# Kernel optimization log

Measured on AMD Instinct MI355X. Metric: run time of the kernel, lower is better.

Reference implementation:

```python
import math
import jax, jax.numpy as jnp
from jax import lax
import numpy as np

B, M, L = 256, 21, 512
P, S, D = 16, 8, 256
NL, EXP, H, LAM = 3, 2, 96, 0.01
T = (L - P) // S + 1  # 63 patches
HID = D * EXP


def _pos_enc():
    pe = np.zeros((T, D), np.float32)
    pos = np.arange(T, dtype=np.float32)[:, None]
    div = np.exp(np.arange(0, D, 2, dtype=np.float32) * (-math.log(10000.0) / D))
    pe[:, 0::2] = np.sin(pos * div)
    pe[:, 1::2] = np.cos(pos * div)
    return jnp.asarray(pe)


def _clin(zr, zi, Wr, Wi, br, bi):
    # faithful to torch: bias br added to both terms of yr (cancels), bi added twice in yi
    yr = (zr @ Wr.T + br) - (zi @ Wi.T + br)
    yi = (zr @ Wi.T + bi) + (zi @ Wr.T + bi)
    return yr, yi


def _softshrink(zr, zi):
    mag = jnp.sqrt(zr * zr + zi * zi)
    scale = jnp.maximum(mag - LAM, 0.0) / (mag + 1e-8) * (mag > LAM).astype(zr.dtype)
    return zr * scale, zi * scale


def _layernorm(x, g, b):
    mu = jnp.mean(x, -1, keepdims=True)
    var = jnp.mean((x - mu) ** 2, -1, keepdims=True)
    return (x - mu) / jnp.sqrt(var + 1e-5) * g + b


def _block(x, p):
    (Tw, Tb, Gew, Geb, Gpw, Gpb,
     H1Wr, H1Wi, H1br, H1bi, H2Wr, H2Wi, H2br, H2bi, lng, lnb) = p
    g = jax.nn.gelu(x @ Gew.T + Geb, approximate=False) @ Gpw.T + Gpb
    zf = jnp.fft.rfft(x, axis=1)  # FFT along time/patch axis T
    zr, zi = zf.real, zf.imag
    zr, zi = _clin(zr, zi, H1Wr, H1Wi, H1br, H1bi)
    zr, zi = _softshrink(zr, zi)
    zr, zi = _clin(zr, zi, H2Wr, H2Wi, H2br, H2bi)
    pt = jnp.fft.irfft(lax.complex(zr, zi), n=x.shape[1], axis=1)
    out = (g * pt) @ Tw.T + Tb
    return _layernorm(out + x, lng, lnb)


def _forward(x, conv_w, conv_b, tp, sp, gate_w, gate_b, proj_w, proj_b):
    # per-instance, per-variable norm over time (biased std, eps on std)
    mean = jnp.mean(x, -1, keepdims=True)
    std = jnp.sqrt(jnp.mean((x - mean) ** 2, -1, keepdims=True))
    xn = (x - mean) / (std + 1e-5)
    patches = lax.conv_general_dilated(xn, conv_w, (S,), 'VALID',
                                       dimension_numbers=('NCH', 'OIH', 'NCH'))
    patches = patches + conv_b[None, :, None]
    h = patches.transpose(0, 2, 1) + _pos_enc()[None]  # (B, T, D)
    t = h
    s = h
    for i in range(NL):
        t = _block(t, tuple(a[i] for a in tp))
        s = _block(s, tuple(a[i] for a in sp))
    gate = jax.nn.sigmoid(t @ gate_w.T + gate_b)
    feat = gate * t + (1.0 - gate) * s
    out = feat.reshape(feat.shape[0], -1) @ proj_w.T + proj_b
    y = out.reshape(-1, M, H) * (std + 1e-5) + mean
    return y


def setup_inputs() -> dict:
    key = jax.random.key(0)
    ks = iter(jax.random.split(key, 64))

    def nrm(shape, scale):
        return jax.random.normal(next(ks), shape, jnp.float32) * scale

    inp = {'x': nrm((B, M, L), 1.0)}
    inp['conv_w'] = nrm((D, M, P), 1.0 / math.sqrt(M * P))
    inp['conv_b'] = jnp.zeros((D,), jnp.float32)

    def layer_params(prefix):
        d = {}
        d[prefix + 'Tw'] = nrm((NL, D, D), 1.0 / math.sqrt(D))
        d[prefix + 'Tb'] = jnp.zeros((NL, D), jnp.float32)
        d[prefix + 'Gew'] = nrm((NL, HID, D), 1.0 / math.sqrt(D))
        d[prefix + 'Geb'] = jnp.zeros((NL, HID), jnp.float32)
        d[prefix + 'Gpw'] = nrm((NL, D, HID), 1.0 / math.sqrt(HID))
        d[prefix + 'Gpb'] = jnp.zeros((NL, D), jnp.float32)
        for hname in ('H1', 'H2'):
            d[prefix + hname + 'Wr'] = nrm((NL, D, D), 1.0 / math.sqrt(D))
            d[prefix + hname + 'Wi'] = nrm((NL, D, D), 1.0 / math.sqrt(D))
            d[prefix + hname + 'br'] = jnp.zeros((NL, D), jnp.float32)
            d[prefix + hname + 'bi'] = jnp.zeros((NL, D), jnp.float32)
        d[prefix + 'lng'] = jnp.ones((NL, D), jnp.float32)
        d[prefix + 'lnb'] = jnp.zeros((NL, D), jnp.float32)
        return d

    inp.update(layer_params('t_'))
    inp.update(layer_params('s_'))
    inp['gate_w'] = nrm((1, D), 1.0 / math.sqrt(D))
    inp['gate_b'] = jnp.zeros((1,), jnp.float32)
    inp['proj_w'] = nrm((M * H, T * D), 1.0 / math.sqrt(T * D))
    inp['proj_b'] = jnp.zeros((M * H,), jnp.float32)
    return inp


def reference(x, conv_w, conv_b,
              t_Tw, t_Tb, t_Gew, t_Geb, t_Gpw, t_Gpb,
              t_H1Wr, t_H1Wi, t_H1br, t_H1bi, t_H2Wr, t_H2Wi, t_H2br, t_H2bi, t_lng, t_lnb,
              s_Tw, s_Tb, s_Gew, s_Geb, s_Gpw, s_Gpb,
              s_H1Wr, s_H1Wi, s_H1br, s_H1bi, s_H2Wr, s_H2Wi, s_H2br, s_H2bi, s_lng, s_lnb,
              gate_w, gate_b, proj_w, proj_b):
    tp = (t_Tw, t_Tb, t_Gew, t_Geb, t_Gpw, t_Gpb,
          t_H1Wr, t_H1Wi, t_H1br, t_H1bi, t_H2Wr, t_H2Wi, t_H2br, t_H2bi, t_lng, t_lnb)
    sp = (s_Tw, s_Tb, s_Gew, s_Geb, s_Gpw, s_Gpb,
          s_H1Wr, s_H1Wi, s_H1br, s_H1bi, s_H2Wr, s_H2Wi, s_H2br, s_H2bi, s_lng, s_lnb)
    return _forward(x, conv_w, conv_b, tp, sp, gate_w, gate_b, proj_w, proj_b)
```

## Files before the change

kernel.cpp:

```cpp
#include <hip/hip_runtime.h>
#include <cstddef>
#include <cstdint>

#define B_    256
#define M_    21
#define L_    512
#define D_    256
#define T_    63
#define F_    32
#define NT_   16128
#define HID_  512
#define KCP_  352
#define H_    96
#define LAM_  0.01f
#define PZ_   12

typedef __attribute__((ext_vector_type(8))) short short8;
typedef __attribute__((ext_vector_type(4))) float f32x4;
typedef unsigned int u32;
typedef const u32 __attribute__((address_space(1)))* gas1_t;
typedef u32 __attribute__((address_space(3)))* las3_t;

__device__ __forceinline__ void async_copy16(const void* g, void* l) {
  __builtin_amdgcn_global_load_lds((gas1_t)g, (las3_t)(uintptr_t)l, 16, 0, 0);
}
__device__ __forceinline__ unsigned short f2bf(float x) {
  unsigned u = __float_as_uint(x);
  return (unsigned short)((u + 0x7FFF + ((u >> 16) & 1)) >> 16);
}
__device__ __forceinline__ float bf2f(unsigned short u) {
  return __uint_as_float(((unsigned)u) << 16);
}
__device__ __forceinline__ float gelu_exact(float v) {
  return 0.5f * v * (1.0f + erff(v * 0.70710678118654752f));
}
__device__ __forceinline__ float block_sum256(float v, float* red4) {
  #pragma unroll
  for (int off = 32; off > 0; off >>= 1) v += __shfl_down(v, off, 64);
  if ((threadIdx.x & 63) == 0) red4[threadIdx.x >> 6] = v;
  __syncthreads();
  float r = red4[0] + red4[1] + red4[2] + red4[3];
  __syncthreads();
  return r;
}
__device__ __forceinline__ float wave_sum(float v) {
  #pragma unroll
  for (int off = 1; off < 64; off <<= 1) v += __shfl_xor(v, off, 64);
  return v;
}

struct CvtEnt { const float* src; unsigned short* dst; int rows, scol, dcol, blk0; };
struct CvtArgs { CvtEnt e[19]; int nent; };
__global__ __launch_bounds__(256) void wprep_kernel(CvtArgs a) {
  int blk = blockIdx.x, e = 0;
  while (e + 1 < a.nent && a.e[e + 1].blk0 <= blk) ++e;
  CvtEnt en = a.e[e];
  int idx = (blk - en.blk0) * 256 + threadIdx.x;
  int total = en.rows * en.dcol;
  if (idx >= total) return;
  int r = idx / en.dcol, c = idx - r * en.dcol;
  float v = (c < en.scol) ? en.src[(size_t)r * en.scol + c] : 0.f;
  en.dst[idx] = f2bf(v);
}

struct CatArgs { const float* wr[12]; const float* wi[12]; };
__global__ __launch_bounds__(256) void wcat_kernel(CatArgs a, unsigned short* dst) {
  int e = blockIdx.x >> 10;
  int idx = ((blockIdx.x & 1023) << 8) + threadIdx.x;
  int r = idx >> 9, c = idx & 511;
  int cp = r >> 1, p = r & 1, d = c >> 1, q = c & 1;
  const float* wr = a.wr[e];
  const float* wi = a.wi[e];
  float v;
  if (p == 0) v = (q == 0) ? wr[cp * 256 + d] : -wi[cp * 256 + d];
  else        v = (q == 0) ? wi[cp * 256 + d] :  wr[cp * 256 + d];
  dst[(size_t)e * 262144 + idx] = f2bf(v);
}

template <int ACT, int OUTBF, int BIASM, int KSTEPS, int CVTA, int CVTW,
          int SHRINK, int MULPT, int SPLITK>
__global__ __launch_bounds__(256) void mm_kernel(
    const void* __restrict__ Av,
    const unsigned short* __restrict__ W0, const unsigned short* __restrict__ W1,
    const float* __restrict__ Wf,
    const float* __restrict__ b0, const float* __restrict__ b1,
    const unsigned short* __restrict__ ptb,
    void* __restrict__ Cv,
    const int K, const int Dout, const int ksteps_rt, const int yhalf, const int prow) {
  __shared__ __align__(16) unsigned short As[128 * 32];
  __shared__ __align__(16) unsigned short Bs[128 * 32];
  const int ksteps = KSTEPS ? KSTEPS : ksteps_rt;
  const int tid = threadIdx.x, w = tid >> 6, lane = tid & 63;
  const int quad = lane >> 4, r16 = lane & 15;
  const int kst = SPLITK ? (int)blockIdx.z * ksteps * 32 : 0;
  const int tower = ((int)blockIdx.y >= yhalf) ? 1 : 0;
  const unsigned short* Wb = tower ? W1 : W0;
  const float* bias = tower ? b1 : b0;

  const unsigned short* Ab = (const unsigned short*)Av;
  const float* Af = (const float*)Av;
  const unsigned short* gA = nullptr;
  unsigned short* lA = As + (w * 32) * 32;
  if (!CVTA) gA = Ab + (size_t)(blockIdx.y * 128 + w * 32 + (lane >> 2)) * K
                     + kst + (lane & 3) * 8;
  const unsigned short* gB = nullptr;
  unsigned short* lB = Bs + (w * 32) * 32;
  if (!CVTW) gB = Wb + (size_t)(blockIdx.x * 128 + w * 32 + (lane >> 2)) * K
                     + kst + (lane & 3) * 8;

  f32x4 acc[4][4];
  #pragma unroll
  for (int i = 0; i < 4; ++i)
    #pragma unroll
    for (int j = 0; j < 4; ++j)
      #pragma unroll
      for (int r = 0; r < 4; ++r) acc[i][j][r] = 0.f;

  for (int ks = 0; ks < ksteps; ++ks) {
    if (!CVTA) {
      async_copy16(gA, lA);
      async_copy16(gA + (size_t)16 * K, lA + 16 * 32);
      gA += 32;
    } else {
      int rowA = tid >> 1, halfk = (tid & 1) << 4;
      const float* asrc = Af + (size_t)((int)blockIdx.y * 128 + rowA) * K + ks * 32 + halfk;
      union { unsigned short u[16]; uint4 q[2]; } pk;
      #pragma unroll
      for (int n = 0; n < 16; n += 4) {
        float4 v = *reinterpret_cast<const float4*>(asrc + n);
        pk.u[n] = f2bf(v.x); pk.u[n + 1] = f2bf(v.y);
        pk.u[n + 2] = f2bf(v.z); pk.u[n + 3] = f2bf(v.w);
      }
      uint4* ad = reinterpret_cast<uint4*>(As + rowA * 32 + halfk);
      ad[0] = pk.q[0]; ad[1] = pk.q[1];
    }
    if (!CVTW) {
      async_copy16(gB, lB);
      async_copy16(gB + (size_t)16 * K, lB + 16 * 32);
      gB += 32;
    } else {
      int rowW = tid >> 1, halfk = (tid & 1) << 4;
      int wrow = blockIdx.x * 128 + rowW;
      if (wrow >= Dout) wrow = Dout - 1;
      const float* wsrc = Wf + (size_t)wrow * K + kst + ks * 32 + halfk;
      union { unsigned short u[16]; uint4 q[2]; } pk;
      #pragma unroll
      for (int n = 0; n < 16; n += 4) {
        float4 v = *reinterpret_cast<const float4*>(wsrc + n);
        pk.u[n] = f2bf(v.x); pk.u[n + 1] = f2bf(v.y);
        pk.u[n + 2] = f2bf(v.z); pk.u[n + 3] = f2bf(v.w);
      }
      uint4* bd = reinterpret_cast<uint4*>(Bs + rowW * 32 + halfk);
      bd[0] = pk.q[0]; bd[1] = pk.q[1];
    }
    __syncthreads();
    const unsigned short* pa = As + (64 * (w >> 1) + r16) * 32 + quad * 8;
    const unsigned short* pb = Bs + (64 * (w & 1) + r16) * 32 + quad * 8;
    short8 af[4], bfv[4];
    #pragma unroll
    for (int i = 0; i < 4; ++i) af[i] = *reinterpret_cast<const short8*>(pa + i * 512);
    #pragma unroll
    for (int j = 0; j < 4; ++j) bfv[j] = *reinterpret_cast<const short8*>(pb + j * 512);
    #pragma unroll
    for (int i = 0; i < 4; ++i)
      #pragma unroll
      for (int j = 0; j < 4; ++j)
        acc[i][j] = __builtin_amdgcn_mfma_f32_16x16x32_bf16(af[i], bfv[j], acc[i][j], 0, 0, 0);
    __syncthreads();
  }

  float* Cf = (float*)Cv;
  unsigned short* Cb = (unsigned short*)Cv;
  if (SPLITK) Cf += (size_t)blockIdx.z * prow * Dout;
  const int colb = blockIdx.x * 128 + 64 * (w & 1) + r16;
  const int rowb = blockIdx.y * 128 + 64 * (w >> 1) + quad * 4;
  #pragma unroll
  for (int j = 0; j < 4; ++j) {
    int col = colb + 16 * j;
    float bv = 0.f;
    if (BIASM == 0) bv = bias[col];
    else if (BIASM == 1) bv = (col & 1) ? 2.0f * bias[col >> 1] : 0.f;
    bool colok = (BIASM != 2) || (col < Dout);
    #pragma unroll
    for (int i = 0; i < 4; ++i) {
      #pragma unroll
      for (int r = 0; r < 4; ++r) {
        int row = rowb + 16 * i + r;
        float v = acc[i][j][r] + bv;
        if (ACT == 1) v = gelu_exact(v);
        if (SHRINK) {
          float o = __shfl_xor(v, 1, 64);
          float mag = sqrtf(v * v + o * o);
          float s = (mag > LAM_) ? (mag - LAM_) / (mag + 1e-8f) : 0.f;
          v *= s;
        }
        if (MULPT) v *= bf2f(ptb[(size_t)row * Dout + col]);
        if (colok) {
          if (OUTBF) Cb[(size_t)row * Dout + col] = f2bf(v);
          else       Cf[(size_t)row * Dout + col] = v;
        }
      }
    }
  }
}

__global__ __launch_bounds__(256) void norm_kernel(const float* __restrict__ x,
    float* __restrict__ xn, float* __restrict__ meanb, float* __restrict__ stdb) {
  __shared__ float red[4];
  int bm = blockIdx.x;
  const float* xr = x + (size_t)bm * L_;
  float v0 = xr[threadIdx.x], v1 = xr[threadIdx.x + 256];
  float mu = block_sum256(v0 + v1, red) * (1.0f / L_);
  float d0 = v0 - mu, d1 = v1 - mu;
  float sd = sqrtf(block_sum256(d0 * d0 + d1 * d1, red) * (1.0f / L_));
  float inv = 1.0f / (sd + 1e-5f);
  float* xo = xn + (size_t)bm * L_;
  xo[threadIdx.x] = d0 * inv;
  xo[threadIdx.x + 256] = d1 * inv;
  if (threadIdx.x == 0) { meanb[bm] = mu; stdb[bm] = sd; }
}

__global__ __launch_bounds__(256) void im2col_kernel(const float* __restrict__ xn,
                                                     unsigned short* __restrict__ im) {
  int row = blockIdx.x;
  int b = row / T_, t = row - b * T_;
  const float* xb = xn + (size_t)b * M_ * L_ + t * 8;
  unsigned short* o = im + (size_t)row * KCP_;
  for (int i = threadIdx.x; i < KCP_; i += 256) {
    float v = 0.f;
    if (i < 336) { int m = i >> 4, p = i & 15; v = xb[m * L_ + p]; }
    o[i] = f2bf(v);
  }
}

__global__ __launch_bounds__(256) void add_pe_kernel(const float* __restrict__ g0,
                                                     float* __restrict__ x32) {
  int row = blockIdx.x, d = threadIdx.x;
  int t = row % T_;
  size_t idx = (size_t)row * D_ + d;
  float freq = expf((float)(d & ~1) * (-9.210340371976184f / 256.0f));
  float ang = (float)t * freq;
  float pe = (d & 1) ? cosf(ang) : sinf(ang);
  float h = g0[idx] + pe;
  x32[idx] = h;
  x32[idx + (size_t)NT_ * D_] = h;
}

__global__ __launch_bounds__(256) void dft_kernel(const float* __restrict__ X,
                                                  unsigned short* __restrict__ Zcat) {
  __shared__ float2 tw[T_ * F_];
  int bt = blockIdx.x, d = threadIdx.x;
  for (int i = threadIdx.x; i < T_ * F_; i += 256) {
    int t = i >> 5, f = i & 31;
    int k = (f * t) % T_;
    float sn, cs;
    sincosf((6.283185307179586f / 63.0f) * (float)k, &sn, &cs);
    tw[i] = make_float2(cs, -sn);
  }
  __syncthreads();
  const float* xb = X + (size_t)bt * T_ * D_ + d;
  float ar[F_], ai[F_];
  #pragma unroll
  for (int f = 0; f < F_; ++f) { ar[f] = 0.f; ai[f] = 0.f; }
  for (int t = 0; t < T_; ++t) {
    float v = xb[(size_t)t * D_];
    const float2* w = &tw[t * F_];
    #pragma unroll
    for (int f = 0; f < F_; ++f) {
      float2 c = w[f];
      ar[f] = fmaf(v, c.x, ar[f]);
      ai[f] = fmaf(v, c.y, ai[f]);
    }
  }
  u32* z = reinterpret_cast<u32*>(Zcat + (size_t)bt * F_ * 512);
  #pragma unroll
  for (int f = 0; f < F_; ++f)
    z[f * 256 + d] = (u32)f2bf(ar[f]) | ((u32)f2bf(ai[f]) << 16);
}

__global__ __launch_bounds__(256) void irfft_kernel(const float* __restrict__ Y,
                                                    unsigned short* __restrict__ ptb) {
  __shared__ float2 tw[T_ * 31];
  int bt = blockIdx.x, d = threadIdx.x;
  for (int i = threadIdx.x; i < T_ * 31; i += 256) {
    int t = i / 31, f = i - t * 31 + 1;
    int k = (f * t) % T_;
    float sn, cs;
    sincosf((6.283185307179586f / 63.0f) * (float)k, &sn, &cs);
    tw[i] = make_float2(cs * (2.0f / 63.0f), -sn * (2.0f / 63.0f));
  }
  __syncthreads();
  const float* yb = Y + (size_t)bt * F_ * 512 + 2 * d;
  float y0 = yb[0] * (1.0f / 63.0f);
  float yr[31], yi[31];
  #pragma unroll
  for (int f = 1; f < F_; ++f) {
    float2 p = *reinterpret_cast<const float2*>(yb + (size_t)f * 512);
    yr[f - 1] = p.x;
    yi[f - 1] = p.y;
  }
  unsigned short* po = ptb + (size_t)bt * T_ * D_ + d;
  for (int t = 0; t < T_; ++t) {
    const float2* w = &tw[t * 31];
    float acc0 = y0, acc1 = 0.f;
    #pragma unroll
    for (int f = 0; f < 31; f += 2) {
      float2 c = w[f];
      acc0 = fmaf(yr[f], c.x, fmaf(yi[f], c.y, acc0));
      if (f + 1 < 31) {
        float2 c1 = w[f + 1];
        acc1 = fmaf(yr[f + 1], c1.x, fmaf(yi[f + 1], c1.y, acc1));
      }
    }
    po[(size_t)t * D_] = f2bf(acc0 + acc1);
  }
}

__global__ __launch_bounds__(256) void ln_kernel(const float* __restrict__ outb,
    float* __restrict__ x, const float* __restrict__ g0, const float* __restrict__ b0,
    const float* __restrict__ g1, const float* __restrict__ b1, int yhalf) {
  int row = blockIdx.x * 4 + (threadIdx.x >> 6);
  int lane = threadIdx.x & 63;
  const float* g = (row >= yhalf) ? g1 : g0;
  const float* b = (row >= yhalf) ? b1 : b0;
  size_t base = (size_t)row * D_ + lane * 4;
  float4 ov = *reinterpret_cast<const float4*>(outb + base);
  float4 xv = *reinterpret_cast<const float4*>(x + base);
  float v0 = ov.x + xv.x, v1 = ov.y + xv.y, v2 = ov.z + xv.z, v3 = ov.w + xv.w;
  float mu = wave_sum(v0 + v1 + v2 + v3) * (1.0f / D_);
  v0 -= mu; v1 -= mu; v2 -= mu; v3 -= mu;
  float var = wave_sum(v0 * v0 + v1 * v1 + v2 * v2 + v3 * v3) * (1.0f / D_);
  float is = rsqrtf(var + 1e-5f);
  float4 gv = *reinterpret_cast<const float4*>(g + lane * 4);
  float4 bv = *reinterpret_cast<const float4*>(b + lane * 4);
  float4 o;
  o.x = v0 * is * gv.x + bv.x;
  o.y = v1 * is * gv.y + bv.y;
  o.z = v2 * is * gv.z + bv.z;
  o.w = v3 * is * gv.w + bv.w;
  *reinterpret_cast<float4*>(x + base) = o;
}

__global__ __launch_bounds__(256) void gate_feat_kernel(const float* __restrict__ x32,
    const float* __restrict__ gw, const float* __restrict__ gb,
    unsigned short* __restrict__ featbf) {
  __shared__ float red[4];
  size_t base = (size_t)blockIdx.x * D_;
  int d = threadIdx.x;
  float tv = x32[base + d];
  float sv = x32[base + (size_t)NT_ * D_ + d];
  float gsum = block_sum256(tv * gw[d], red) + gb[0];
  float gate = 1.0f / (1.0f + expf(-gsum));
  featbf[base + d] = f2bf(gate * tv + (1.0f - gate) * sv);
}

__global__ __launch_bounds__(256) void final_kernel(const float* __restrict__ part,
    const float* __restrict__ pb, const float* __restrict__ stdb,
    const float* __restrict__ meanb, float* __restrict__ y) {
  int i = blockIdx.x * 256 + threadIdx.x;
  float acc = 0.f;
  #pragma unroll
  for (int z = 0; z < PZ_; ++z) acc += part[(size_t)z * 516096 + i];
  int b = i / 2016;
  int col = i - b * 2016;
  int m = col / H_;
  float sc = stdb[b * M_ + m] + 1e-5f;
  y[i] = (acc + pb[col]) * sc + meanb[b * M_ + m];
}

extern "C" void kernel_launch(void* const* d_in, const int* in_sizes, int n_in,
                              void* d_out, int out_size, void* d_ws, size_t ws_size,
                              hipStream_t stream) {
  const float* x      = (const float*)d_in[0];
  const float* conv_w = (const float*)d_in[1];
  const float* conv_b = (const float*)d_in[2];
  const float* tP[16];
  const float* sP[16];
  for (int i = 0; i < 16; ++i) tP[i] = (const float*)d_in[3 + i];
  for (int i = 0; i < 16; ++i) sP[i] = (const float*)d_in[19 + i];
  const float* gate_w = (const float*)d_in[35];
  const float* gate_b = (const float*)d_in[36];
  const float* proj_w = (const float*)d_in[37];
  const float* proj_b = (const float*)d_in[38];
  float* out = (float*)d_out;

  float* ws    = (float*)d_ws;
  float* x32   = ws;
  unsigned short* wb = (unsigned short*)(x32 + 8257536);
  float* meanb = x32 + 8257536 + 2600960;
  float* stdb  = meanb + 5376;
  float* R1    = stdb + 5376 + 16;
  float* R2    = R1 + 8388608;

  unsigned short* im2colB = (unsigned short*)R1;
  unsigned short* Zcat    = (unsigned short*)R1;
  unsigned short* Ycat1   = (unsigned short*)(R1 + 4194304);
  unsigned short* ptb     = (unsigned short*)(R1 + 4194304);
  unsigned short* gp      = (unsigned short*)R1;
  unsigned short* featbf  = (unsigned short*)R1;

  float* xn     = R2;
  float* g0buf  = R2;
  float* Ycat2f = R2;
  unsigned short* hidB = (unsigned short*)R2;
  float* outb   = R2;
  float* part   = R2;

  unsigned short* convW = wb;
  unsigned short* sets  = wb + 90112;
  unsigned short* catW  = wb + 90112 + 1966080;

  CvtArgs ca; int blk0 = 0, ne = 0;
  auto add_ent = [&](const float* s, unsigned short* d, int rows, int scol, int dcol) {
    ca.e[ne].src = s; ca.e[ne].dst = d; ca.e[ne].rows = rows;
    ca.e[ne].scol = scol; ca.e[ne].dcol = dcol; ca.e[ne].blk0 = blk0;
    blk0 += (rows * dcol + 255) / 256; ++ne;
  };
  add_ent(conv_w, convW, 256, 336, 352);
  for (int tw = 0; tw < 2; ++tw) {
    const float** Pp = tw ? (const float**)sP : (const float**)tP;
    for (int l = 0; l < 3; ++l) {
      unsigned short* sb = sets + (size_t)(tw * 3 + l) * 327680;
      add_ent(Pp[2] + (size_t)l * 131072, sb,          512, 256, 256);
      add_ent(Pp[4] + (size_t)l * 131072, sb + 131072, 256, 512, 512);
      add_ent(Pp[0] + (size_t)l * 65536,  sb + 262144, 256, 256, 256);
    }
  }
  ca.nent = ne;
  wprep_kernel<<<blk0, 256, 0, stream>>>(ca);

  CatArgs cat;
  for (int tw = 0; tw < 2; ++tw) {
    const float** Pp = tw ? (const float**)sP : (const float**)tP;
    for (int l = 0; l < 3; ++l) {
      int e0 = (tw * 3 + l) * 2;
      cat.wr[e0]     = Pp[6]  + (size_t)l * 65536;
      cat.wi[e0]     = Pp[7]  + (size_t)l * 65536;
      cat.wr[e0 + 1] = Pp[10] + (size_t)l * 65536;
      cat.wi[e0 + 1] = Pp[11] + (size_t)l * 65536;
    }
  }
  wcat_kernel<<<12 * 1024, 256, 0, stream>>>(cat, catW);

  norm_kernel<<<B_ * M_, 256, 0, stream>>>(x, xn, meanb, stdb);
  im2col_kernel<<<NT_, 256, 0, stream>>>(xn, im2colB);
  mm_kernel<0, 0, 0, 11, 0, 0, 0, 0, 0><<<dim3(2, 126), 256, 0, stream>>>(
      im2colB, convW, convW, nullptr, conv_b, conv_b, nullptr, g0buf,
      KCP_, 256, 0, 1 << 30, 0);
  add_pe_kernel<<<NT_, 256, 0, stream>>>(g0buf, x32);

  for (int l = 0; l < 3; ++l) {
    unsigned short* st0 = sets + (size_t)l * 327680;
    unsigned short* st1 = sets + (size_t)(3 + l) * 327680;
    unsigned short* c1t0 = catW + (size_t)((0 + l) * 2) * 262144;
    unsigned short* c2t0 = c1t0 + 262144;
    unsigned short* c1t1 = catW + (size_t)((3 + l) * 2) * 262144;
    unsigned short* c2t1 = c1t1 + 262144;

    dft_kernel<<<2 * B_, 256, 0, stream>>>(x32, Zcat);
    mm_kernel<0, 1, 1, 16, 0, 0, 1, 0, 0><<<dim3(4, 128), 256, 0, stream>>>(
        Zcat, c1t0, c1t1, nullptr, tP[9] + (size_t)l * D_, sP[9] + (size_t)l * D_,
        nullptr, Ycat1, 512, 512, 0, 64, 0);
    mm_kernel<0, 0, 1, 16, 0, 0, 0, 0, 0><<<dim3(4, 128), 256, 0, stream>>>(
        Ycat1, c2t0, c2t1, nullptr, tP[13] + (size_t)l * D_, sP[13] + (size_t)l * D_,
        nullptr, Ycat2f, 512, 512, 0, 64, 0);
    irfft_kernel<<<2 * B_, 256, 0, stream>>>(Ycat2f, ptb);
    mm_kernel<1, 1, 0, 8, 1, 0, 0, 0, 0><<<dim3(4, 252), 256, 0, stream>>>(
        x32, st0, st1, nullptr, tP[3] + (size_t)l * HID_, sP[3] + (size_t)l * HID_,
        nullptr, hidB, 256, 512, 0, 126, 0);
    mm_kernel<0, 1, 0, 16, 0, 0, 0, 1, 0><<<dim3(2, 252), 256, 0, stream>>>(
        hidB, st0 + 131072, st1 + 131072, nullptr,
        tP[5] + (size_t)l * D_, sP[5] + (size_t)l * D_, ptb, gp, 512, 256, 0, 126, 0);
    mm_kernel<0, 0, 0, 8, 0, 0, 0, 0, 0><<<dim3(2, 252), 256, 0, stream>>>(
        gp, st0 + 262144, st1 + 262144, nullptr,
        tP[1] + (size_t)l * D_, sP[1] + (size_t)l * D_, nullptr, outb, 256, 256, 0, 126, 0);
    ln_kernel<<<2 * NT_ / 4, 256, 0, stream>>>(outb, x32,
        tP[14] + (size_t)l * D_, tP[15] + (size_t)l * D_,
        sP[14] + (size_t)l * D_, sP[15] + (size_t)l * D_, NT_);
  }

  gate_feat_kernel<<<NT_, 256, 0, stream>>>(x32, gate_w, gate_b, featbf);
  mm_kernel<0, 0, 2, 0, 0, 1, 0, 0, 1><<<dim3(16, 2, PZ_), 256, 0, stream>>>(
      featbf, nullptr, nullptr, proj_w, nullptr, nullptr, nullptr, part,
      NT_, 2016, 504 / PZ_, 1 << 30, 256);
  final_kernel<<<2016, 256, 0, stream>>>(part, proj_b, stdb, meanb, out);
}
```

Measured before the change: 1.067 ms.

## Deepen GEMM K-tile to 64, store second spectral GEMM in bf16, vectorize gate kernel

```diff
diff --git a/kernel.cpp b/kernel.cpp
--- a/kernel.cpp
+++ b/kernel.cpp
@@ -13,7 +13,7 @@
 #define KCP_  352
 #define H_    96
 #define LAM_  0.01f
-#define PZ_   12
+#define PZ_   14
 
 typedef __attribute__((ext_vector_type(8))) short short8;
 typedef __attribute__((ext_vector_type(4))) float f32x4;
@@ -78,7 +78,7 @@
 }
 
 template <int ACT, int OUTBF, int BIASM, int KSTEPS, int CVTA, int CVTW,
-          int SHRINK, int MULPT, int SPLITK>
+          int SHRINK, int MULPT, int SPLITK, int BK>
 __global__ __launch_bounds__(256) void mm_kernel(
     const void* __restrict__ Av,
     const unsigned short* __restrict__ W0, const unsigned short* __restrict__ W1,
@@ -87,12 +87,13 @@
     const unsigned short* __restrict__ ptb,
     void* __restrict__ Cv,
     const int K, const int Dout, const int ksteps_rt, const int yhalf, const int prow) {
-  __shared__ __align__(16) unsigned short As[128 * 32];
-  __shared__ __align__(16) unsigned short Bs[128 * 32];
+  constexpr int NP = BK / 32;
+  __shared__ __align__(16) unsigned short As[NP * 128 * 32];
+  __shared__ __align__(16) unsigned short Bs[NP * 128 * 32];
   const int ksteps = KSTEPS ? KSTEPS : ksteps_rt;
   const int tid = threadIdx.x, w = tid >> 6, lane = tid & 63;
   const int quad = lane >> 4, r16 = lane & 15;
-  const int kst = SPLITK ? (int)blockIdx.z * ksteps * 32 : 0;
+  const int kst = SPLITK ? (int)blockIdx.z * ksteps * BK : 0;
   const int tower = ((int)blockIdx.y >= yhalf) ? 1 : 0;
   const unsigned short* Wb = tower ? W1 : W0;
   const float* bias = tower ? b1 : b0;
@@ -107,6 +108,8 @@
   unsigned short* lB = Bs + (w * 32) * 32;
   if (!CVTW) gB = Wb + (size_t)(blockIdx.x * 128 + w * 32 + (lane >> 2)) * K
                      + kst + (lane & 3) * 8;
+  const int crow = tid >> 3;
+  const int ck4  = (tid & 7) << 2;
 
   f32x4 acc[4][4];
   #pragma unroll
@@ -118,54 +121,62 @@
 
   for (int ks = 0; ks < ksteps; ++ks) {
     if (!CVTA) {
-      async_copy16(gA, lA);
-      async_copy16(gA + (size_t)16 * K, lA + 16 * 32);
-      gA += 32;
+      #pragma unroll
+      for (int p = 0; p < NP; ++p) {
+        async_copy16(gA + p * 32, lA + p * 4096);
+        async_copy16(gA + (size_t)16 * K + p * 32, lA + p * 4096 + 16 * 32);
+      }
+      gA += BK;
     } else {
-      int rowA = tid >> 1, halfk = (tid & 1) << 4;
-      const float* asrc = Af + (size_t)((int)blockIdx.y * 128 + rowA) * K + ks * 32 + halfk;
-      union { unsigned short u[16]; uint4 q[2]; } pk;
-      #pragma unroll
-      for (int n = 0; n < 16; n += 4) {
-        float4 v = *reinterpret_cast<const float4*>(asrc + n);
-        pk.u[n] = f2bf(v.x); pk.u[n + 1] = f2bf(v.y);
-        pk.u[n + 2] = f2bf(v.z); pk.u[n + 3] = f2bf(v.w);
+      #pragma unroll
+      for (int p = 0; p < NP; ++p)
+        #pragma unroll
+        for (int rr = 0; rr < 4; ++rr) {
+          int row128 = crow + 32 * rr;
+          const float* asrc = Af + (size_t)((int)blockIdx.y * 128 + row128) * K
+                                 + ks * BK + p * 32 + ck4;
+          float4 v = *reinterpret_cast<const float4*>(asrc);
+          ushort4 o; o.x = f2bf(v.x); o.y = f2bf(v.y); o.z = f2bf(v.z); o.w = f2bf(v.w);
+          *reinterpret_cast<ushort4*>(As + p * 4096 + row128 * 32 + ck4) = o;
+        }
+    }
+    if (!CVTW) {
+      #pragma unroll
+      for (int p = 0; p < NP; ++p) {
+        async_copy16(gB + p * 32, lB + p * 4096);
+        async_copy16(gB + (size_t)16 * K + p * 32, lB + p * 4096 + 16 * 32);
       }
-      uint4* ad = reinterpret_cast<uint4*>(As + rowA * 32 + halfk);
-      ad[0] = pk.q[0]; ad[1] = pk.q[1];
-    }
-    if (!CVTW) {
-      async_copy16(gB, lB);
-      async_copy16(gB + (size_t)16 * K, lB + 16 * 32);
-      gB += 32;
+      gB += BK;
     } else {
-      int rowW = tid >> 1, halfk = (tid & 1) << 4;
-      int wrow = blockIdx.x * 128 + rowW;
-      if (wrow >= Dout) wrow = Dout - 1;
-      const float* wsrc = Wf + (size_t)wrow * K + kst + ks * 32 + halfk;
-      union { unsigned short u[16]; uint4 q[2]; } pk;
-      #pragma unroll
-      for (int n = 0; n < 16; n += 4) {
-        float4 v = *reinterpret_cast<const float4*>(wsrc + n);
-        pk.u[n] = f2bf(v.x); pk.u[n + 1] = f2bf(v.y);
-        pk.u[n + 2] = f2bf(v.z); pk.u[n + 3] = f2bf(v.w);
-      }
-      uint4* bd = reinterpret_cast<uint4*>(Bs + rowW * 32 + halfk);
-      bd[0] = pk.q[0]; bd[1] = pk.q[1];
+      #pragma unroll
+      for (int p = 0; p < NP; ++p)
+        #pragma unroll
+        for (int rr = 0; rr < 4; ++rr) {
+          int row128 = crow + 32 * rr;
+          int wrow = blockIdx.x * 128 + row128;
+          if (wrow >= Dout) wrow = Dout - 1;
+          const float* wsrc = Wf + (size_t)wrow * K + kst + ks * BK + p * 32 + ck4;
+          float4 v = *reinterpret_cast<const float4*>(wsrc);
+          ushort4 o; o.x = f2bf(v.x); o.y = f2bf(v.y); o.z = f2bf(v.z); o.w = f2bf(v.w);
+          *reinterpret_cast<ushort4*>(Bs + p * 4096 + row128 * 32 + ck4) = o;
+        }
     }
     __syncthreads();
-    const unsigned short* pa = As + (64 * (w >> 1) + r16) * 32 + quad * 8;
-    const unsigned short* pb = Bs + (64 * (w & 1) + r16) * 32 + quad * 8;
-    short8 af[4], bfv[4];
     #pragma unroll
-    for (int i = 0; i < 4; ++i) af[i] = *reinterpret_cast<const short8*>(pa + i * 512);
-    #pragma unroll
-    for (int j = 0; j < 4; ++j) bfv[j] = *reinterpret_cast<const short8*>(pb + j * 512);
-    #pragma unroll
-    for (int i = 0; i < 4; ++i)
-      #pragma unroll
-      for (int j = 0; j < 4; ++j)
-        acc[i][j] = __builtin_amdgcn_mfma_f32_16x16x32_bf16(af[i], bfv[j], acc[i][j], 0, 0, 0);
+    for (int p = 0; p < NP; ++p) {
+      const unsigned short* pa = As + p * 4096 + (64 * (w >> 1) + r16) * 32 + quad * 8;
+      const unsigned short* pb = Bs + p * 4096 + (64 * (w & 1) + r16) * 32 + quad * 8;
+      short8 af[4], bfv[4];
+      #pragma unroll
+      for (int i = 0; i < 4; ++i) af[i] = *reinterpret_cast<const short8*>(pa + i * 512);
+      #pragma unroll
+      for (int j = 0; j < 4; ++j) bfv[j] = *reinterpret_cast<const short8*>(pb + j * 512);
+      #pragma unroll
+      for (int i = 0; i < 4; ++i)
+        #pragma unroll
+        for (int j = 0; j < 4; ++j)
+          acc[i][j] = __builtin_amdgcn_mfma_f32_16x16x32_bf16(af[i], bfv[j], acc[i][j], 0, 0, 0);
+    }
     __syncthreads();
   }
 
@@ -278,7 +289,7 @@
     z[f * 256 + d] = (u32)f2bf(ar[f]) | ((u32)f2bf(ai[f]) << 16);
 }
 
-__global__ __launch_bounds__(256) void irfft_kernel(const float* __restrict__ Y,
+__global__ __launch_bounds__(256) void irfft_kernel(const unsigned short* __restrict__ Y,
                                                     unsigned short* __restrict__ ptb) {
   __shared__ float2 tw[T_ * 31];
   int bt = blockIdx.x, d = threadIdx.x;
@@ -290,14 +301,14 @@
     tw[i] = make_float2(cs * (2.0f / 63.0f), -sn * (2.0f / 63.0f));
   }
   __syncthreads();
-  const float* yb = Y + (size_t)bt * F_ * 512 + 2 * d;
-  float y0 = yb[0] * (1.0f / 63.0f);
+  const unsigned short* yb = Y + (size_t)bt * F_ * 512 + 2 * d;
+  float y0 = bf2f(yb[0]) * (1.0f / 63.0f);
   float yr[31], yi[31];
   #pragma unroll
   for (int f = 1; f < F_; ++f) {
-    float2 p = *reinterpret_cast<const float2*>(yb + (size_t)f * 512);
-    yr[f - 1] = p.x;
-    yi[f - 1] = p.y;
+    u32 p = *reinterpret_cast<const u32*>(yb + (size_t)f * 512);
+    yr[f - 1] = bf2f((unsigned short)(p & 0xffff));
+    yi[f - 1] = bf2f((unsigned short)(p >> 16));
   }
   unsigned short* po = ptb + (size_t)bt * T_ * D_ + d;
   for (int t = 0; t < T_; ++t) {
@@ -344,14 +355,20 @@
 __global__ __launch_bounds__(256) void gate_feat_kernel(const float* __restrict__ x32,
     const float* __restrict__ gw, const float* __restrict__ gb,
     unsigned short* __restrict__ featbf) {
-  __shared__ float red[4];
-  size_t base = (size_t)blockIdx.x * D_;
-  int d = threadIdx.x;
-  float tv = x32[base + d];
-  float sv = x32[base + (size_t)NT_ * D_ + d];
-  float gsum = block_sum256(tv * gw[d], red) + gb[0];
-  float gate = 1.0f / (1.0f + expf(-gsum));
-  featbf[base + d] = f2bf(gate * tv + (1.0f - gate) * sv);
+  int row = blockIdx.x * 4 + (threadIdx.x >> 6);
+  int lane = threadIdx.x & 63;
+  size_t base = (size_t)row * D_ + lane * 4;
+  float4 tv = *reinterpret_cast<const float4*>(x32 + base);
+  float4 sv = *reinterpret_cast<const float4*>(x32 + base + (size_t)NT_ * D_);
+  float4 gv = *reinterpret_cast<const float4*>(gw + lane * 4);
+  float dot = wave_sum(tv.x * gv.x + tv.y * gv.y + tv.z * gv.z + tv.w * gv.w) + gb[0];
+  float gate = 1.0f / (1.0f + expf(-dot));
+  ushort4 o;
+  o.x = f2bf(gate * tv.x + (1.0f - gate) * sv.x);
+  o.y = f2bf(gate * tv.y + (1.0f - gate) * sv.y);
+  o.z = f2bf(gate * tv.z + (1.0f - gate) * sv.z);
+  o.w = f2bf(gate * tv.w + (1.0f - gate) * sv.w);
+  *reinterpret_cast<ushort4*>(featbf + base) = o;
 }
 
 __global__ __launch_bounds__(256) void final_kernel(const float* __restrict__ part,
@@ -401,7 +418,7 @@
 
   float* xn     = R2;
   float* g0buf  = R2;
-  float* Ycat2f = R2;
+  unsigned short* Ycat2b = (unsigned short*)R2;
   unsigned short* hidB = (unsigned short*)R2;
   float* outb   = R2;
   float* part   = R2;
@@ -444,7 +461,7 @@
 
   norm_kernel<<<B_ * M_, 256, 0, stream>>>(x, xn, meanb, stdb);
   im2col_kernel<<<NT_, 256, 0, stream>>>(xn, im2colB);
-  mm_kernel<0, 0, 0, 11, 0, 0, 0, 0, 0><<<dim3(2, 126), 256, 0, stream>>>(
+  mm_kernel<0, 0, 0, 11, 0, 0, 0, 0, 0, 32><<<dim3(2, 126), 256, 0, stream>>>(
       im2colB, convW, convW, nullptr, conv_b, conv_b, nullptr, g0buf,
       KCP_, 256, 0, 1 << 30, 0);
   add_pe_kernel<<<NT_, 256, 0, stream>>>(g0buf, x32);
@@ -458,20 +475,20 @@
     unsigned short* c2t1 = c1t1 + 262144;
 
     dft_kernel<<<2 * B_, 256, 0, stream>>>(x32, Zcat);
-    mm_kernel<0, 1, 1, 16, 0, 0, 1, 0, 0><<<dim3(4, 128), 256, 0, stream>>>(
+    mm_kernel<0, 1, 1, 8, 0, 0, 1, 0, 0, 64><<<dim3(4, 128), 256, 0, stream>>>(
         Zcat, c1t0, c1t1, nullptr, tP[9] + (size_t)l * D_, sP[9] + (size_t)l * D_,
         nullptr, Ycat1, 512, 512, 0, 64, 0);
-    mm_kernel<0, 0, 1, 16, 0, 0, 0, 0, 0><<<dim3(4, 128), 256, 0, stream>>>(
+    mm_kernel<0, 1, 1, 8, 0, 0, 0, 0, 0, 64><<<dim3(4, 128), 256, 0, stream>>>(
         Ycat1, c2t0, c2t1, nullptr, tP[13] + (size_t)l * D_, sP[13] + (size_t)l * D_,
-        nullptr, Ycat2f, 512, 512, 0, 64, 0);
-    irfft_kernel<<<2 * B_, 256, 0, stream>>>(Ycat2f, ptb);
-    mm_kernel<1, 1, 0, 8, 1, 0, 0, 0, 0><<<dim3(4, 252), 256, 0, stream>>>(
+        nullptr, Ycat2b, 512, 512, 0, 64, 0);
+    irfft_kernel<<<2 * B_, 256, 0, stream>>>(Ycat2b, ptb);
+    mm_kernel<1, 1, 0, 4, 1, 0, 0, 0, 0, 64><<<dim3(4, 252), 256, 0, stream>>>(
         x32, st0, st1, nullptr, tP[3] + (size_t)l * HID_, sP[3] + (size_t)l * HID_,
         nullptr, hidB, 256, 512, 0, 126, 0);
-    mm_kernel<0, 1, 0, 16, 0, 0, 0, 1, 0><<<dim3(2, 252), 256, 0, stream>>>(
+    mm_kernel<0, 1, 0, 8, 0, 0, 0, 1, 0, 64><<<dim3(2, 252), 256, 0, stream>>>(
         hidB, st0 + 131072, st1 + 131072, nullptr,
         tP[5] + (size_t)l * D_, sP[5] + (size_t)l * D_, ptb, gp, 512, 256, 0, 126, 0);
-    mm_kernel<0, 0, 0, 8, 0, 0, 0, 0, 0><<<dim3(2, 252), 256, 0, stream>>>(
+    mm_kernel<0, 0, 0, 4, 0, 0, 0, 0, 0, 64><<<dim3(2, 252), 256, 0, stream>>>(
         gp, st0 + 262144, st1 + 262144, nullptr,
         tP[1] + (size_t)l * D_, sP[1] + (size_t)l * D_, nullptr, outb, 256, 256, 0, 126, 0);
     ln_kernel<<<2 * NT_ / 4, 256, 0, stream>>>(outb, x32,
@@ -479,8 +496,8 @@
         sP[14] + (size_t)l * D_, sP[15] + (size_t)l * D_, NT_);
   }
 
-  gate_feat_kernel<<<NT_, 256, 0, stream>>>(x32, gate_w, gate_b, featbf);
-  mm_kernel<0, 0, 2, 0, 0, 1, 0, 0, 1><<<dim3(16, 2, PZ_), 256, 0, stream>>>(
+  gate_feat_kernel<<<NT_ / 4, 256, 0, stream>>>(x32, gate_w, gate_b, featbf);
+  mm_kernel<0, 0, 2, 0, 0, 1, 0, 0, 1, 32><<<dim3(16, 2, PZ_), 256, 0, stream>>>(
       featbf, nullptr, nullptr, proj_w, nullptr, nullptr, nullptr, part,
       NT_, 2016, 504 / PZ_, 1 << 30, 256);
   final_kernel<<<2016, 256, 0, stream>>>(part, proj_b, stdb, meanb, out);
```

Measured after the change: 1.022 ms. 1.04x faster.
